# Kernel tuning notes

Measured on AMD Instinct MI355X. Metric: run time of the kernel, lower is better.

Reference implementation:

```python
import jax, jax.numpy as jnp
import numpy as np

N, D, R, DR, H, L = 6000, 128, 1000, 128, 2, 2
MAXN = 1.0 - 4e-3  # Poincare ball projection boundary (c=1)


def _norm(x):
    return jnp.clip(jnp.linalg.norm(x, axis=-1, keepdims=True), 1e-15)


def proj(x):
    n = _norm(x)
    return jnp.where(n > MAXN, x / n * MAXN, x)


def expmap0(u):
    n = _norm(u)
    return proj(jnp.tanh(n) * u / n)


def logmap0(p):
    n = _norm(p)
    return jnp.arctanh(jnp.minimum(n, 1.0 - 1e-7)) * p / n


def mobius_add(x, y):
    x2 = jnp.sum(x * x, -1, keepdims=True)
    y2 = jnp.sum(y * y, -1, keepdims=True)
    xy = jnp.sum(x * y, -1, keepdims=True)
    num = (1 + 2 * xy + y2) * x + (1 - x2) * y
    den = 1 + 2 * xy + x2 * y2
    return num / jnp.clip(den, 1e-15)


def hgc_layer(x, adj, W, b):
    # HypLinear (mobius matvec + hyperbolic bias), HypAgg (tangent-space SpMM), HypAct (relu)
    mv = proj(expmap0(logmap0(x) @ W.T))
    h = proj(mobius_add(mv, proj(expmap0(b))))
    h = proj(expmap0(adj @ logmap0(h)))
    return proj(expmap0(jax.nn.relu(logmap0(h))))


def gat_layer(x, adj, W, a_src, a_dst):
    h = jnp.einsum('nd,hde->hne', x, W)                 # [H,N,D]
    es = jnp.einsum('hne,he->hn', h, a_src)
    ed = jnp.einsum('hne,he->hn', h, a_dst)
    e = jax.nn.leaky_relu(es[:, :, None] + ed[:, None, :], 0.2)  # [H,N,N]
    att = jax.nn.softmax(jnp.where(adj[None] > 0, e, -1e9), axis=-1)
    out = jnp.einsum('hnm,hme->hne', att, h).mean(0)    # head-average -> [N,D]
    return jax.nn.elu(out)


def mha(x, Wq, Wk, Wv, Wfc, g, b):
    # Transformer-style MHA with residual + LayerNorm; x: [N, Lr, D]
    Nn, Lr, _ = x.shape
    split = lambda y: y.reshape(Nn, Lr, H, D).transpose(0, 2, 1, 3)
    q, k, v = split(x @ Wq), split(x @ Wk), split(x @ Wv)
    attn = jax.nn.softmax(jnp.einsum('nhld,nhmd->nhlm', q, k) / jnp.sqrt(jnp.float32(D)), -1)
    o = jnp.einsum('nhlm,nhmd->nhld', attn, v).transpose(0, 2, 1, 3).reshape(Nn, Lr, H * D)
    o = o @ Wfc + x
    mu = o.mean(-1, keepdims=True)
    var = o.var(-1, keepdims=True)
    return g * (o - mu) / jnp.sqrt(var + 1e-6) + b


def _forward(ent_sr, ent_tg, rel_sr, rel_tg, adj_sr, adj_tg, rel_adj_sr, rel_adj_tg,
             gat_W, gat_a_src, gat_a_dst, Wq, Wk, Wv, Wfc, ln_g, ln_b, hgc_W, hgc_b):
    # Relation Aggregator: sparse mm + rowsum normalization
    def rel_agg(radj, remb):
        return (radj @ remb) / radj.sum(-1, keepdims=True)
    sr_rel = rel_agg(rel_adj_sr, rel_sr)
    tg_rel = rel_agg(rel_adj_tg, rel_tg)

    # Attentive Neighbor Aggregator + multi-range fusion (res=True -> range = L+1)
    def branch(x, adj):
        outs, h = [x], x
        for i in range(L):
            h = gat_layer(h, adj, gat_W[i], gat_a_src[i], gat_a_dst[i])
            h = h / jnp.clip(_norm(h), 1e-12)  # F.normalize(dim=1)
            outs.append(h)
        seq = jnp.stack(outs, axis=1)  # [N, L+1, D]
        return mha(seq, Wq, Wk, Wv, Wfc, ln_g, ln_b).mean(1)
    sr = branch(ent_sr, adj_sr)
    tg = branch(ent_tg, adj_tg)

    # Hyperbolic encoder (proj_tan0 is identity for PoincareBall)
    def encode(x, adj):
        h = expmap0(x)
        for i in range(2):
            h = hgc_layer(h, adj, hgc_W[i], hgc_b[i])
        return logmap0(h)
    hs = ent_sr + encode(ent_sr, adj_sr)
    ht = ent_tg + encode(ent_tg, adj_tg)

    return (jnp.concatenate([sr, sr_rel], -1), jnp.concatenate([tg, tg_rel], -1),
            jnp.concatenate([hs, sr_rel], -1), jnp.concatenate([ht, tg_rel], -1))


def setup_inputs() -> dict:
    key = jax.random.key(0)
    ks = jax.random.split(key, 24)

    def make_adj(k):
        m = jax.random.bernoulli(k, 32.0 / N, (N, N)) | jnp.eye(N, dtype=bool)
        a = m.astype(jnp.float32)
        return a / a.sum(-1, keepdims=True)

    def make_rel_adj(k1, k2):
        m = jax.random.bernoulli(k1, 5.0 / R, (N, R)).astype(jnp.float32)
        idx = jax.random.randint(k2, (N,), 0, R)
        return m.at[jnp.arange(N), idx].set(1.0)  # guarantee positive rowsum

    return {
        'ent_sr': 0.02 * jax.random.normal(ks[0], (N, D)),
        'ent_tg': 0.02 * jax.random.normal(ks[1], (N, D)),
        'rel_sr': 0.02 * jax.random.normal(ks[2], (R, DR)),
        'rel_tg': 0.02 * jax.random.normal(ks[3], (R, DR)),
        'adj_sr': make_adj(ks[4]),
        'adj_tg': make_adj(ks[5]),
        'rel_adj_sr': make_rel_adj(ks[6], ks[7]),
        'rel_adj_tg': make_rel_adj(ks[8], ks[9]),
        'gat_W': 0.1 * jax.random.normal(ks[10], (L, H, D, D)),
        'gat_a_src': 0.1 * jax.random.normal(ks[11], (L, H, D)),
        'gat_a_dst': 0.1 * jax.random.normal(ks[12], (L, H, D)),
        'Wq': 0.05 * jax.random.normal(ks[13], (D, H * D)),
        'Wk': 0.05 * jax.random.normal(ks[14], (D, H * D)),
        'Wv': 0.05 * jax.random.normal(ks[15], (D, H * D)),
        'Wfc': 0.05 * jax.random.normal(ks[16], (H * D, D)),
        'ln_g': jnp.ones((D,)),
        'ln_b': jnp.zeros((D,)),
        'hgc_W': 0.05 * jax.random.normal(ks[17], (2, D, D)),
        'hgc_b': 0.01 * jax.random.normal(ks[18], (2, D)),
    }


def reference(ent_sr, ent_tg, rel_sr, rel_tg, adj_sr, adj_tg, rel_adj_sr, rel_adj_tg,
              gat_W, gat_a_src, gat_a_dst, Wq, Wk, Wv, Wfc, ln_g, ln_b, hgc_W, hgc_b):
    return _forward(ent_sr, ent_tg, rel_sr, rel_tg, adj_sr, adj_tg, rel_adj_sr, rel_adj_tg,
                    gat_W, gat_a_src, gat_a_dst, Wq, Wk, Wv, Wfc, ln_g, ln_b, hgc_W, hgc_b)
```

## Files before the change

### kernel.cpp

```cpp
#include <hip/hip_runtime.h>
#include <hip/hip_bf16.h>
#include <math.h>

#define NN   6000
#define N2   12000
#define DD   128
#define RR   1000
#define CAP  96
#define CAPR 48
#define MAXN_F 0.996f

typedef short  bf16x8 __attribute__((ext_vector_type(8)));
typedef float  f32x4  __attribute__((ext_vector_type(4)));

__device__ int      g_dt[19];
__device__ unsigned g_csri[N2 * CAP];
__device__ int      g_cnt[N2];
__device__ float    g_seq[N2 * 3 * DD];
__device__ unsigned short g_seqb[N2 * 3 * DD];
__device__ unsigned short g_hhb[N2 * 256];
__device__ float    g_es[2][N2];
__device__ float    g_ed[2][N2];
__device__ unsigned short g_qkvb[(size_t)N2 * 3 * 768];
__device__ unsigned short g_ob[(size_t)N2 * 3 * 256];
__device__ float    g_fc[N2 * 3 * DD];
__device__ float    g_t[N2 * DD];
__device__ float    g_t2[N2 * DD];
__device__ float    g_hb[2][DD];
__device__ float    g_hb2[2];
__device__ unsigned short g_WgatT[2][256 * DD];
__device__ unsigned short g_WqkvT[768 * DD];
__device__ unsigned short g_WfcT[DD * 256];
__device__ float    g_WhgcT[2][DD * DD];

__device__ __forceinline__ float ldin(const void* p, size_t i, int bf) {
    if (bf) return __uint_as_float(((unsigned)((const unsigned short*)p)[i]) << 16);
    return ((const float*)p)[i];
}
__device__ __forceinline__ unsigned short f2b(float f) {
    unsigned u = __float_as_uint(f);
    u += 0x7FFFu + ((u >> 16) & 1u);
    return (unsigned short)(u >> 16);
}
__device__ __forceinline__ float b2f(unsigned short b) {
    return __uint_as_float(((unsigned)b) << 16);
}
__device__ __forceinline__ float adjval(int c) {
    return b2f(f2b(1.0f / (float)c));
}

__device__ __forceinline__ float wsum(float v) {
    #pragma unroll
// ... 7 lines not shown
}
__device__ __forceinline__ float b128sum(float v, float* r4) {
    v = wsum(v);
    if ((threadIdx.x & 63) == 0) r4[threadIdx.x >> 6] = v;
    __syncthreads();
    float r = r4[0] + r4[1];
    __syncthreads();
    return r;
}
__device__ __forceinline__ void b128sum2(float v0, float v1, float* r4, float& o0, float& o1) {
    v0 = wsum(v0); v1 = wsum(v1);
    int w = threadIdx.x >> 6;
    if ((threadIdx.x & 63) == 0) { r4[w * 2] = v0; r4[w * 2 + 1] = v1; }
    __syncthreads();
    o0 = r4[0] + r4[2]; o1 = r4[1] + r4[3];
    __syncthreads();
}
__device__ __forceinline__ void b128max2(float v0, float v1, float* r4, float& o0, float& o1) {
    v0 = wmax(v0); v1 = wmax(v1);
    int w = threadIdx.x >> 6;
    if ((threadIdx.x & 63) == 0) { r4[w * 2] = v0; r4[w * 2 + 1] = v1; }
    __syncthreads();
    o0 = fmaxf(r4[0], r4[2]); o1 = fmaxf(r4[1], r4[3]);
    __syncthreads();
}

struct P19 { const void* p[19]; };

__global__ void detect_all(P19 ptrs) {
    const int sizes[19] = {768000,768000,128000,128000,36000000,36000000,6000000,6000000,
                           65536,512,512,32768,32768,32768,32768,128,128,32768,256};
    int slot = blockIdx.x;
    const unsigned* p = (const unsigned*)ptrs.p[slot];
    __shared__ int votes[2];
    if (threadIdx.x == 0) { votes[0] = 0; votes[1] = 0; }
    __syncthreads();
    int nwords = sizes[slot] / 2;
    if (nwords > 0) {
        int nsamp = nwords < 4096 ? nwords : 4096;
        int stride = nwords / nsamp; if (stride < 1) stride = 1;
        for (int s = threadIdx.x; s < nsamp; s += blockDim.x) {
            unsigned lo = p[(size_t)s * stride] & 0xFFFFu;
            if (lo) {
                unsigned e = (lo >> 7) & 0xFFu;
                if (e >= 100u && e <= 140u) atomicAdd(&votes[1], 1);
                else                        atomicAdd(&votes[0], 1);
            }
        }
    }
    __syncthreads();
    if (threadIdx.x == 0) g_dt[slot] = (votes[1] > votes[0]) ? 1 : 0;
}

__global__ void prep_weights(const void* gatW, const void* Wq, const void* Wk, const void* Wv,
                             const void* Wfc, const void* hgcW) {
    int stride = gridDim.x * blockDim.x;
    int base = blockIdx.x * blockDim.x + threadIdx.x;
    const int b8 = g_dt[8], b11 = g_dt[11], b12 = g_dt[12], b13 = g_dt[13],
              b14 = g_dt[14], b17 = g_dt[17];
    for (int i = base; i < 65536; i += stride) {
        int e = i & 127, d = (i >> 7) & 127, h = (i >> 14) & 1, l = (i >> 15) & 1;
        g_WgatT[l][(h * 128 + e) * DD + d] = f2b(ldin(gatW, i, b8));
    }
    for (int i = base; i < 32768; i += stride) {
        int d = i >> 8, e = i & 255;
        g_WqkvT[(size_t)e * DD + d]         = f2b(ldin(Wq, i, b11));
        g_WqkvT[(size_t)(256 + e) * DD + d] = f2b(ldin(Wk, i, b12));
        g_WqkvT[(size_t)(512 + e) * DD + d] = f2b(ldin(Wv, i, b13));
    }
    for (int i = base; i < 32768; i += stride) {
        int e = i >> 7, dd = i & 127;
        g_WfcT[dd * 256 + e] = f2b(ldin(Wfc, i, b14));
    }
    for (int i = base; i < 32768; i += stride) {
        int j = i & 127, d = (i >> 7) & 127, l = i >> 14;
        g_WhgcT[l][j * 128 + d] = ldin(hgcW, i, b17);
    }
}

template<bool OUT_BF16>
__global__ __launch_bounds__(256) void gemm_mfma(const unsigned short* __restrict__ A, int lda,
                                                 const unsigned short* __restrict__ Bt, int ldb,
                                                 void* __restrict__ C, int ldc, int M, int K) {
    __shared__ __align__(16) unsigned short As[16 * 128 * 8];
    __shared__ __align__(16) unsigned short Bs[16 * 128 * 8];
    int bm = blockIdx.y * 128, bn = blockIdx.x * 128;
    int tid = threadIdx.x;
    int lane = tid & 63, w = tid >> 6;
    int q = lane >> 4, ln = lane & 15;
    f32x4 acc[8][2] = {};
    for (int k0 = 0; k0 < K; k0 += 128) {
        if (k0 > 0) __syncthreads();
        #pragma unroll
        for (int i = 0; i < 8; i++) {
            int combo = w * 8 + i;
            int c = combo >> 1, half = combo & 1;
            int r = half * 64 + lane;
            int gm = bm + r; if (gm >= M) gm = M - 1;
            *(uint4*)&As[(c * 128 + r) * 8] =
// ... 13 lines not shown
                acc[mt][1] = __builtin_amdgcn_mfma_f32_16x16x32_bf16(af, bf1, acc[mt][1], 0, 0, 0);
            }
        }
    }
    #pragma unroll
    for (int mt = 0; mt < 8; mt++) {
        #pragma unroll
        for (int nt = 0; nt < 2; nt++) {
            int gcol = bn + w * 32 + nt * 16 + ln;
            #pragma unroll
            for (int r = 0; r < 4; r++) {
                int grow = bm + mt * 16 + q * 4 + r;
                if (grow < M) {
                    if (OUT_BF16)
                        ((unsigned short*)C)[(size_t)grow * ldc + gcol] = f2b(acc[mt][nt][r]);
                    else
                        ((float*)C)[(size_t)grow * ldc + gcol] = acc[mt][nt][r];
                }
            }
        }
    }
}

__global__ __launch_bounds__(256) void scan_one(const void* __restrict__ A, int which) {
    int row = (blockIdx.x << 2) | (threadIdx.x >> 6);
    int lane = threadIdx.x & 63;
    if (row >= NN) return;
    int gn = which * NN + row;
    unsigned long long below = (1ull << lane) - 1ull;
    int base = 0;
    if (g_dt[4 + which]) {
        const uint4* p = (const uint4*)((const unsigned short*)A + (size_t)row * NN);
        uint4 cur = p[lane];
        for (int it = 0; it < 12; it++) {
            int idx = it * 64 + lane;
            uint4 nxt = {0u, 0u, 0u, 0u};
            if (it < 11) { int ni = idx + 64; if (ni < 750) nxt = p[ni]; }
            unsigned w4[4] = {cur.x, cur.y, cur.z, cur.w};
            #pragma unroll
            for (int h = 0; h < 4; h++) {
                #pragma unroll
                for (int s = 0; s < 2; s++) {
                    unsigned v16 = s ? (w4[h] >> 16) : (w4[h] & 0xFFFFu);
                    bool pr = v16 && !(v16 & 0x8000u);
                    unsigned long long m = __ballot(pr);
                    if (m) {
                        if (pr) {
                            int pos = base + __popcll(m & below);
                            if (pos < CAP)
                                g_csri[(size_t)gn * CAP + pos] = (unsigned)(idx * 8 + h * 2 + s);
                        }
                        base += __popcll(m);
                    }
                }
            }
            cur = nxt;
        }
    } else {
        const float4* p = (const float4*)((const float*)A + (size_t)row * NN);
        float4 cur = p[lane];
        for (int it = 0; it < 24; it++) {
            int idx = it * 64 + lane;
            float4 nxt = {0.f, 0.f, 0.f, 0.f};
            if (it < 23) { int ni = idx + 64; if (ni < 1500) nxt = p[ni]; }
            float e4[4] = {cur.x, cur.y, cur.z, cur.w};
            #pragma unroll
            for (int h = 0; h < 4; h++) {
                bool pr = e4[h] > 0.f;
                unsigned long long m = __ballot(pr);
                if (m) {
                    if (pr) {
                        int pos = base + __popcll(m & below);
                        if (pos < CAP)
                            g_csri[(size_t)gn * CAP + pos] = (unsigned)(idx * 4 + h);
                    }
                    base += __popcll(m);
                }
            }
            cur = nxt;
        }
    }
    if (lane == 0) g_cnt[gn] = min(base, CAP);
}

__global__ void rel_agg_kernel(const void* __restrict__ ra0, const void* __restrict__ ra1,
                               const void* __restrict__ re0, const void* __restrict__ re1,
                               float* __restrict__ out) {
    int n = blockIdx.x, d = threadIdx.x;
    int which = n >= NN ? 1 : 0;
    const void* radj = which ? ra1 : ra0;
    const void* rel  = which ? re1 : re0;
    const int bfa = g_dt[6 + which], bfr = g_dt[2 + which];
    int row = n - which * NN;
    __shared__ int list[CAPR];
    __shared__ int cs;
    if (d == 0) cs = 0;
    __syncthreads();
    if (bfa) {
        const uint4* p = (const uint4*)((const unsigned short*)radj + (size_t)row * RR);
        for (int i = d; i < RR / 8; i += 128) {
            uint4 w4 = p[i];
            unsigned ws[4] = {w4.x, w4.y, w4.z, w4.w};
            #pragma unroll
            for (int h = 0; h < 4; h++) {
                unsigned lo = ws[h] & 0xFFFFu, hi = ws[h] >> 16;
                if (lo && !(lo & 0x8000u)) { int q = atomicAdd(&cs, 1); if (q < CAPR) list[q] = i * 8 + h * 2; }
                if (hi && !(hi & 0x8000u)) { int q = atomicAdd(&cs, 1); if (q < CAPR) list[q] = i * 8 + h * 2 + 1; }
            }
        }
    } else {
        const float4* p = (const float4*)((const float*)radj + (size_t)row * RR);
        for (int i = d; i < RR / 4; i += 128) {
            float4 w4 = p[i];
            float vs[4] = {w4.x, w4.y, w4.z, w4.w};
            #pragma unroll
            for (int h = 0; h < 4; h++)
                if (vs[h] > 0.f) { int q = atomicAdd(&cs, 1); if (q < CAPR) list[q] = i * 4 + h; }
        }
    }
    __syncthreads();
    int c = min(cs, CAPR);
    float acc = 0.f;
    for (int j = 0; j < c; j++) acc += ldin(rel, (size_t)list[j] * DD + d, bfr);
    float r = c ? acc / (float)c : 0.f;
    out[(size_t)n * 256 + 128 + d] = r;
    out[(size_t)(2 * NN + n) * 256 + 128 + d] = r;
}

__device__ __forceinline__ float hgc_lin_core(float* u, float* r4, int layer, int d) {
    float mv = 0.f;
    #pragma unroll 4
    for (int j = 0; j < DD; j++) mv = fmaf(g_WhgcT[layer][j * 128 + d], u[j], mv);
    float ss2 = b128sum(mv * mv, r4);
    float nm = fmaxf(sqrtf(ss2), 1e-15f);
    float t2 = tanhf(nm);
    float x = t2 / nm * mv;
    float xn = t2;
    if (t2 > MAXN_F) { x *= MAXN_F / t2; xn = MAXN_F; }
    float y = g_hb[layer][d];
    float x2 = xn * xn;
    float y2 = g_hb2[layer];
    float xy = b128sum(x * y, r4);
    float num = (1.f + 2.f * xy + y2) * x + (1.f - x2) * y;
    float den = 1.f + 2.f * xy + x2 * y2;
    den = (fabsf(den) < 1e-15f) ? 1e-15f : den;
    float hv2 = num / den;
    float s3 = b128sum(hv2 * hv2, r4);
    float nn = fmaxf(sqrtf(s3), 1e-15f);
    if (nn > MAXN_F) { hv2 *= MAXN_F / nn; nn = MAXN_F; }
    return atanhf(fminf(nn, 1.f - 1e-7f)) / nn * hv2;
}

__device__ __forceinline__ float hgc_agg_core(const float* tin, int n, int which, float* r4,
                                              int d, unsigned* sidx) {
    int c = min(g_cnt[n], CAP);
    if (d < c)
        sidx[d] = (g_csri[(size_t)n * CAP + d] + (unsigned)(which * NN)) * 128u + (unsigned)d;
    __syncthreads();
    float acc = 0.f;
    int j = 0;
    for (; j + 4 <= c; j += 4) {
        float v0 = tin[(size_t)sidx[j]];
        float v1 = tin[(size_t)sidx[j + 1]];
        float v2 = tin[(size_t)sidx[j + 2]];
        float v3 = tin[(size_t)sidx[j + 3]];
        acc += (v0 + v1) + (v2 + v3);
    }
    for (; j < c; j++) acc += tin[(size_t)sidx[j]];
    acc *= (c > 0) ? adjval(c) : 0.f;
    __syncthreads();
    float ss = b128sum(acc * acc, r4);
    float nm = fmaxf(sqrtf(ss), 1e-15f);
    float t = tanhf(nm);
    float x = t / nm * acc;
    float xn = t;
    if (t > MAXN_F) { x *= MAXN_F / t; xn = MAXN_F; }
    float u = atanhf(fminf(xn, 1.f - 1e-7f)) / fmaxf(xn, 1e-15f) * x;
    u = fmaxf(u, 0.f);
    float ss2 = b128sum(u * u, r4);
    float nm2 = fmaxf(sqrtf(ss2), 1e-15f);
    float t2 = tanhf(nm2);
    float x2 = t2 / nm2 * u;
    float xn2 = t2;
    if (t2 > MAXN_F) { x2 *= MAXN_F / t2; xn2 = MAXN_F; }
    return atanhf(fminf(xn2, 1.f - 1e-7f)) / fmaxf(xn2, 1e-15f) * x2;
}

__global__ void hgc_bias(const void* __restrict__ hgc_b) {
    int i = blockIdx.x, d = threadIdx.x;
    __shared__ float r4[4];
    float bv = ldin(hgc_b, (size_t)i * DD + d, g_dt[18]);
    float ss = b128sum(bv * bv, r4);
    float nrm = fmaxf(sqrtf(ss), 1e-15f);
    float t = tanhf(nrm);
    float v = t / nrm * bv;
    float vn = t;
    if (t > MAXN_F) { v *= MAXN_F / t; vn = MAXN_F; }
    g_hb[i][d] = v;
    if (d == 0) g_hb2[i] = vn * vn;
}

__global__ void ent_init(const void* __restrict__ e0, const void* __restrict__ e1) {
    int n = blockIdx.x, d = threadIdx.x;
    int which = n >= NN ? 1 : 0;
    __shared__ float r4[4];
    __shared__ float u[128];
    float x = ldin(which ? e1 : e0, (size_t)(n - which * NN) * DD + d, g_dt[which]);
    g_seq[(size_t)n * 384 + d] = x;
    g_seqb[(size_t)n * 384 + d] = f2b(x);
    float ss = b128sum(x * x, r4);
    float nrm = fmaxf(sqrtf(ss), 1e-15f);
    float t = tanhf(nrm);
    float scale = t / nrm;
    float hn = t;
    if (t > MAXN_F) { scale *= MAXN_F / t; hn = MAXN_F; }
    u[d] = atanhf(fminf(hn, 1.f - 1e-7f)) / fmaxf(hn, 1e-15f) * (scale * x);
    __syncthreads();
    g_t[(size_t)n * DD + d] = hgc_lin_core(u, r4, 0, d);
}

__global__ __launch_bounds__(256) void gat_scores(int layer, const void* __restrict__ a_src,
                                                  const void* __restrict__ a_dst) {
    int n = blockIdx.x, tid = threadIdx.x;
    int h = tid >> 7, e = tid & 127;
    const int bfs = g_dt[9], bfd = g_dt[10];
    __shared__ float r8[8];
    float hv = b2f(g_hhb[(size_t)n * 256 + tid]);
    size_t abase = ((size_t)layer * 2 + h) * DD;
    float vs = wsum(hv * ldin(a_src, abase + e, bfs));
    float vd = wsum(hv * ldin(a_dst, abase + e, bfd));
    int w = tid >> 6;
    if ((tid & 63) == 0) { r8[w * 2] = vs; r8[w * 2 + 1] = vd; }
    __syncthreads();
    if (tid == 0)   { g_es[0][n] = r8[0] + r8[2]; g_ed[0][n] = r8[1] + r8[3]; }
    if (tid == 128) { g_es[1][n] = r8[4] + r8[6]; g_ed[1][n] = r8[5] + r8[7]; }
}

__global__ void gat_attn(int layer) {
    int n = blockIdx.x, d = threadIdx.x;
    int which = n >= NN ? 1 : 0;
    int c = min(g_cnt[n], CAP);
    __shared__ float w0s[CAP], w1s[CAP];
    __shared__ unsigned bases[CAP];
// ... 31 lines not shown
        accHi = fmaf(g1, b2f((unsigned short)(v1 >> 16)), accHi);
        accLo = fmaf(g2, b2f((unsigned short)(v2 & 0xFFFFu)), accLo);
        accHi = fmaf(g2, b2f((unsigned short)(v2 >> 16)), accHi);
        accLo = fmaf(g3, b2f((unsigned short)(v3 & 0xFFFFu)), accLo);
        accHi = fmaf(g3, b2f((unsigned short)(v3 >> 16)), accHi);
    }
    for (; j < c; j++) {
        unsigned wv = hh32[(size_t)bases[j] + d];
        float wgt = wsrc[j];
        accLo = fmaf(wgt, b2f((unsigned short)(wv & 0xFFFFu)), accLo);
        accHi = fmaf(wgt, b2f((unsigned short)(wv >> 16)), accHi);
    }
    sh[2 * d] = accLo; sh[2 * d + 1] = accHi;
    __syncthreads();
    float o = (c > 0) ? 0.5f * (sh[d] + sh[128 + d]) : 0.f;
    o = o > 0.f ? o : expm1f(o);
    __syncthreads();
    float ss = b128sum(o * o, r4);
    float r = o / fmaxf(sqrtf(ss), 1e-12f);
    g_seq[(size_t)n * 384 + (layer + 1) * 128 + d] = r;
    g_seqb[(size_t)n * 384 + (layer + 1) * 128 + d] = f2b(r);
}

__global__ __launch_bounds__(256) void mha_attn() {
    int n = blockIdx.x, tid = threadIdx.x;
    __shared__ float qs[3][256], ks[3][256], vs[3][256], os[3][256];
    __shared__ float att[2][3][3];
    const unsigned* src = (const unsigned*)(g_qkvb + (size_t)n * 3 * 768);
    for (int t = tid; t < 1152; t += 256) {
        unsigned wv = src[t];
        int l = t / 384, r = t - l * 384;
        int sec = r >> 7, e2 = (r & 127) * 2;
        float f0 = b2f((unsigned short)(wv & 0xFFFFu));
        float f1 = b2f((unsigned short)(wv >> 16));
        float* dstp = (sec == 0) ? qs[l] : (sec == 1) ? ks[l] : vs[l];
        dstp[e2] = f0; dstp[e2 + 1] = f1;
    }
    __syncthreads();
    if (tid < 144) {
        int g = tid >> 3, sub = tid & 7;
        int h = g / 9, lm = g % 9, l = lm / 3, m = lm % 3;
        int d0 = h * 128 + sub * 16;
        float acc = 0.f;
        #pragma unroll
        for (int k = 0; k < 16; k++) acc += qs[l][d0 + k] * ks[m][d0 + k];
        #pragma unroll
        for (int o = 1; o < 8; o <<= 1) acc += __shfl_xor(acc, o, 8);
        if (sub == 0) att[h][l][m] = acc * 0.08838834764831845f;
    }
    __syncthreads();
    if (tid < 6) {
        int h = tid / 3, l = tid % 3;
        float mx = fmaxf(att[h][l][0], fmaxf(att[h][l][1], att[h][l][2]));
        float e0 = expf(att[h][l][0] - mx), e1 = expf(att[h][l][1] - mx), e2 = expf(att[h][l][2] - mx);
        float s = fmaxf(e0 + e1 + e2, 1e-30f);
        att[h][l][0] = e0 / s; att[h][l][1] = e1 / s; att[h][l][2] = e2 / s;
    }
    __syncthreads();
    for (int t = tid; t < 768; t += 256) {
        int l = t >> 8, e = t & 255, h = e >> 7;
        os[l][e] = att[h][l][0] * vs[0][e] + att[h][l][1] * vs[1][e] + att[h][l][2] * vs[2][e];
    }
    __syncthreads();
    unsigned* dst = (unsigned*)(g_ob + (size_t)n * 3 * 256);
    for (int t = tid; t < 384; t += 256) {
        int l = t / 128, e2 = (t % 128) * 2;
        dst[t] = (unsigned)f2b(os[l][e2]) | ((unsigned)f2b(os[l][e2 + 1]) << 16);
    }
}

__global__ void mha_out(const void* __restrict__ g, const void* __restrict__ b,
                        float* __restrict__ out) {
    int n = blockIdx.x, d = threadIdx.x;
    const int bg = g_dt[15], bb = g_dt[16];
    __shared__ float r4[4];
    float ool[3], mu[3], rstd[3];
    #pragma unroll
    for (int l = 0; l < 3; l++)
        ool[l] = g_fc[(size_t)(n * 3 + l) * 128 + d] + g_seq[(size_t)(n * 3 + l) * 128 + d];
    #pragma unroll
    for (int l = 0; l < 3; l++) {
        float s, ss;
        b128sum2(ool[l], ool[l] * ool[l], r4, s, ss);
        mu[l] = s / 128.f;
        rstd[l] = rsqrtf(ss / 128.f - mu[l] * mu[l] + 1e-6f);
    }
    float acc = 0.f;
    #pragma unroll
    for (int l = 0; l < 3; l++) acc += (ool[l] - mu[l]) * rstd[l];
    out[(size_t)n * 256 + d] = ldin(g, d, bg) * (acc / 3.f) + ldin(b, d, bb);
}

__global__ void hgc_mid() {
    int n = blockIdx.x, d = threadIdx.x;
    int which = n >= NN ? 1 : 0;
    __shared__ float r4[4];
    __shared__ float u[128];
    __shared__ unsigned sidx[CAP];
    float u3 = hgc_agg_core(g_t, n, which, r4, d, sidx);
    u[d] = u3;
    __syncthreads();
    g_t2[(size_t)n * DD + d] = hgc_lin_core(u, r4, 1, d);
}

__global__ void hgc_fin(const void* __restrict__ e0, const void* __restrict__ e1,
                        float* __restrict__ out) {
    int n = blockIdx.x, d = threadIdx.x;
    int which = n >= NN ? 1 : 0;
    __shared__ float r4[4];
    __shared__ unsigned sidx[CAP];
    float u3 = hgc_agg_core(g_t2, n, which, r4, d, sidx);
    float ev = ldin(which ? e1 : e0, (size_t)(n - which * NN) * DD + d, g_dt[which]);
    out[(size_t)(2 * NN + n) * 256 + d] = ev + u3;
}

extern "C" void kernel_launch(void* const* d_in, const int* in_sizes, int n_in,
                              void* d_out, int out_size, void* d_ws, size_t ws_size,
                              hipStream_t stream) {
    const void* ent_sr = d_in[0];
    const void* ent_tg = d_in[1];
    const void* rel_sr = d_in[2];
    const void* rel_tg = d_in[3];
    const void* adj_sr = d_in[4];
    const void* adj_tg = d_in[5];
    const void* rel_adj_sr = d_in[6];
    const void* rel_adj_tg = d_in[7];
    const void* gat_W     = d_in[8];
    const void* gat_a_src = d_in[9];
    const void* gat_a_dst = d_in[10];
    const void* Wq  = d_in[11];
    const void* Wk  = d_in[12];
    const void* Wv  = d_in[13];
    const void* Wfc = d_in[14];
    const void* ln_g = d_in[15];
    const void* ln_b = d_in[16];
    const void* hgc_W = d_in[17];
    const void* hgc_b = d_in[18];

    float* out = (float*)d_out;

    unsigned short *p_seqb, *p_hhb, *p_qkvb, *p_ob, *p_WgatT, *p_WqkvT, *p_WfcT;
    float *p_fc;
    hipGetSymbolAddress((void**)&p_seqb,  HIP_SYMBOL(g_seqb));
    hipGetSymbolAddress((void**)&p_hhb,   HIP_SYMBOL(g_hhb));
    hipGetSymbolAddress((void**)&p_qkvb,  HIP_SYMBOL(g_qkvb));
    hipGetSymbolAddress((void**)&p_ob,    HIP_SYMBOL(g_ob));
    hipGetSymbolAddress((void**)&p_WgatT, HIP_SYMBOL(g_WgatT));
    hipGetSymbolAddress((void**)&p_WqkvT, HIP_SYMBOL(g_WqkvT));
    hipGetSymbolAddress((void**)&p_WfcT,  HIP_SYMBOL(g_WfcT));
    hipGetSymbolAddress((void**)&p_fc,    HIP_SYMBOL(g_fc));

    P19 ptrs;
    for (int i = 0; i < 19; i++) ptrs.p[i] = d_in[i];
    detect_all<<<19, 256, 0, stream>>>(ptrs);

    scan_one<<<NN / 4, 256, 0, stream>>>(adj_sr, 0);

    prep_weights<<<128, 256, 0, stream>>>(gat_W, Wq, Wk, Wv, Wfc, hgc_W);
    rel_agg_kernel<<<N2, 128, 0, stream>>>(rel_adj_sr, rel_adj_tg, rel_sr, rel_tg, out);
    hgc_bias<<<2, 128, 0, stream>>>(hgc_b);
    ent_init<<<N2, 128, 0, stream>>>(ent_sr, ent_tg);

    gemm_mfma<true><<<dim3(2, 94), 256, 0, stream>>>(
        p_seqb, 384, p_WgatT, DD, p_hhb, 256, N2, 128);
    gat_scores<<<N2, 256, 0, stream>>>(0, gat_a_src, gat_a_dst);

    scan_one<<<NN / 4, 256, 0, stream>>>(adj_tg, 1);

    gat_attn<<<N2, 128, 0, stream>>>(0);
    gemm_mfma<true><<<dim3(2, 94), 256, 0, stream>>>(
        p_seqb + 128, 384, p_WgatT + (size_t)256 * DD, DD, p_hhb, 256, N2, 128);
    gat_scores<<<N2, 256, 0, stream>>>(1, gat_a_src, gat_a_dst);
    gat_attn<<<N2, 128, 0, stream>>>(1);

    gemm_mfma<true><<<dim3(6, 282), 256, 0, stream>>>(
        p_seqb, 128, p_WqkvT, DD, p_qkvb, 768, N2 * 3, 128);
    mha_attn<<<N2, 256, 0, stream>>>();
    gemm_mfma<false><<<dim3(1, 282), 256, 0, stream>>>(
        p_ob, 256, p_WfcT, 256, p_fc, 128, N2 * 3, 256);
    mha_out<<<N2, 128, 0, stream>>>(ln_g, ln_b, out);

    hgc_mid<<<N2, 128, 0, stream>>>();
    hgc_fin<<<N2, 128, 0, stream>>>(ent_sr, ent_tg, out);
}
```

Measured before the change: 707.5 us.

## Merge independent front, attention and HGC stages into horizontally fused mega-kernels

Combines the adjacency scans, relation aggregation, entity init, first HGC linear layer and weight prep into one block-partitioned kernel. The MHA attention is merged with the second HGC aggregation/linear stage, and the LayerNorm output with the final HGC aggregation. HGC work now packs two nodes per 256-thread block and computes the hyperbolic bias inline instead of in a separate kernel. The aim is fewer launches and better overlap of independent work, at the cost of heavier blocks, more shared memory per block, and redundant bias computation in every block.

```diff
diff --git a/kernel.cpp b/kernel.cpp
--- a/kernel.cpp
+++ b/kernel.cpp
@@ -26,8 +26,6 @@
 __device__ float    g_fc[N2 * 3 * DD];
 __device__ float    g_t[N2 * DD];
 __device__ float    g_t2[N2 * DD];
-__device__ float    g_hb[2][DD];
-__device__ float    g_hb2[2];
 __device__ unsigned short g_WgatT[2][256 * DD];
 __device__ unsigned short g_WqkvT[768 * DD];
 __device__ unsigned short g_WfcT[DD * 256];
@@ -81,6 +79,26 @@
     if ((threadIdx.x & 63) == 0) { r4[w * 2] = v0; r4[w * 2 + 1] = v1; }
     __syncthreads();
     o0 = fmaxf(r4[0], r4[2]); o1 = fmaxf(r4[1], r4[3]);
+    __syncthreads();
+}
+__device__ __forceinline__ float h128sum(float v, float* r8) {
+    v = wsum(v);
+    int w = threadIdx.x >> 6;
+    if ((threadIdx.x & 63) == 0) r8[w] = v;
+    __syncthreads();
+    int h = threadIdx.x >> 7;
+    float r = r8[2 * h] + r8[2 * h + 1];
+    __syncthreads();
+    return r;
+}
+__device__ __forceinline__ void h128sum2(float v0, float v1, float* r8, float& o0, float& o1) {
+    v0 = wsum(v0); v1 = wsum(v1);
+    int w = threadIdx.x >> 6;
+    if ((threadIdx.x & 63) == 0) { r8[w * 2] = v0; r8[w * 2 + 1] = v1; }
+    __syncthreads();
+    int h = threadIdx.x >> 7;
+    o0 = r8[4 * h] + r8[4 * h + 2];
+    o1 = r8[4 * h + 1] + r8[4 * h + 3];
     __syncthreads();
 }
 
@@ -111,29 +129,224 @@
     if (threadIdx.x == 0) g_dt[slot] = (votes[1] > votes[0]) ? 1 : 0;
 }
 
-__global__ void prep_weights(const void* gatW, const void* Wq, const void* Wk, const void* Wv,
-                             const void* Wfc, const void* hgcW) {
-    int stride = gridDim.x * blockDim.x;
-    int base = blockIdx.x * blockDim.x + threadIdx.x;
-    const int b8 = g_dt[8], b11 = g_dt[11], b12 = g_dt[12], b13 = g_dt[13],
-              b14 = g_dt[14], b17 = g_dt[17];
-    for (int i = base; i < 65536; i += stride) {
-        int e = i & 127, d = (i >> 7) & 127, h = (i >> 14) & 1, l = (i >> 15) & 1;
-        g_WgatT[l][(h * 128 + e) * DD + d] = f2b(ldin(gatW, i, b8));
-    }
-    for (int i = base; i < 32768; i += stride) {
-        int d = i >> 8, e = i & 255;
-        g_WqkvT[(size_t)e * DD + d]         = f2b(ldin(Wq, i, b11));
-        g_WqkvT[(size_t)(256 + e) * DD + d] = f2b(ldin(Wk, i, b12));
-        g_WqkvT[(size_t)(512 + e) * DD + d] = f2b(ldin(Wv, i, b13));
-    }
-    for (int i = base; i < 32768; i += stride) {
-        int e = i >> 7, dd = i & 127;
-        g_WfcT[dd * 256 + e] = f2b(ldin(Wfc, i, b14));
-    }
-    for (int i = base; i < 32768; i += stride) {
-        int j = i & 127, d = (i >> 7) & 127, l = i >> 14;
-        g_WhgcT[l][j * 128 + d] = ldin(hgcW, i, b17);
+__device__ __forceinline__ float bias_inline(const void* hgc_b, int layer, int d, float* r8,
+                                             float& y2) {
+    float bv = ldin(hgc_b, (size_t)layer * DD + d, g_dt[18]);
+    float ss = h128sum(bv * bv, r8);
+    float nrm = fmaxf(sqrtf(ss), 1e-15f);
+    float t = tanhf(nrm);
+    float v = t / nrm * bv;
+    float vn = t;
+    if (t > MAXN_F) { v *= MAXN_F / t; vn = MAXN_F; }
+    y2 = vn * vn;
+    return v;
+}
+
+__device__ __forceinline__ float hgc_lin_h(const float* uh, float* r8, int layer, int d,
+                                           float y, float y2) {
+    float mv = 0.f;
+    #pragma unroll 4
+    for (int j = 0; j < DD; j++) mv = fmaf(g_WhgcT[layer][j * 128 + d], uh[j], mv);
+    float ss2 = h128sum(mv * mv, r8);
+    float nm = fmaxf(sqrtf(ss2), 1e-15f);
+    float t2 = tanhf(nm);
+    float x = t2 / nm * mv;
+    float xn = t2;
+    if (t2 > MAXN_F) { x *= MAXN_F / t2; xn = MAXN_F; }
+    float x2 = xn * xn;
+    float xy = h128sum(x * y, r8);
+    float num = (1.f + 2.f * xy + y2) * x + (1.f - x2) * y;
+    float den = 1.f + 2.f * xy + x2 * y2;
+    den = (fabsf(den) < 1e-15f) ? 1e-15f : den;
+    float hv2 = num / den;
+    float s3 = h128sum(hv2 * hv2, r8);
+    float nn = fmaxf(sqrtf(s3), 1e-15f);
+    if (nn > MAXN_F) { hv2 *= MAXN_F / nn; nn = MAXN_F; }
+    return atanhf(fminf(nn, 1.f - 1e-7f)) / nn * hv2;
+}
+
+__device__ __forceinline__ float hgc_agg_h(const float* tin, int n, int which, float* r8,
+                                           int d, unsigned* sidxh) {
+    int c = min(g_cnt[n], CAP);
+    if (d < c)
+        sidxh[d] = (g_csri[(size_t)n * CAP + d] + (unsigned)(which * NN)) * 128u + (unsigned)d;
+    __syncthreads();
+    float acc = 0.f;
+    int j = 0;
+    for (; j + 4 <= c; j += 4) {
+        float v0 = tin[(size_t)sidxh[j]];
+        float v1 = tin[(size_t)sidxh[j + 1]];
+        float v2 = tin[(size_t)sidxh[j + 2]];
+        float v3 = tin[(size_t)sidxh[j + 3]];
+        acc += (v0 + v1) + (v2 + v3);
+    }
+    for (; j < c; j++) acc += tin[(size_t)sidxh[j]];
+    acc *= (c > 0) ? adjval(c) : 0.f;
+    __syncthreads();
+    float ss = h128sum(acc * acc, r8);
+    float nm = fmaxf(sqrtf(ss), 1e-15f);
+    float t = tanhf(nm);
+    float x = t / nm * acc;
+    float xn = t;
+    if (t > MAXN_F) { x *= MAXN_F / t; xn = MAXN_F; }
+    float u = atanhf(fminf(xn, 1.f - 1e-7f)) / fmaxf(xn, 1e-15f) * x;
+    u = fmaxf(u, 0.f);
+    float ss2 = h128sum(u * u, r8);
+    float nm2 = fmaxf(sqrtf(ss2), 1e-15f);
+    float t2 = tanhf(nm2);
+    float x2 = t2 / nm2 * u;
+    float xn2 = t2;
+    if (t2 > MAXN_F) { x2 *= MAXN_F / t2; xn2 = MAXN_F; }
+    return atanhf(fminf(xn2, 1.f - 1e-7f)) / fmaxf(xn2, 1e-15f) * x2;
+}
+
+__global__ __launch_bounds__(256) void front_mega(P19 in, float* __restrict__ out) {
+    int b = blockIdx.x;
+    int tid = threadIdx.x;
+    if (b < 3000) {
+        int which = b >= 1500 ? 1 : 0;
+        int row = ((which ? b - 1500 : b) << 2) | (tid >> 6);
+        int lane = tid & 63;
+        const void* A = in.p[4 + which];
+        int gn = which * NN + row;
+        unsigned long long below = (1ull << lane) - 1ull;
+        int base = 0;
+        if (g_dt[4 + which]) {
+            const uint4* p = (const uint4*)((const unsigned short*)A + (size_t)row * NN);
+            uint4 cur = p[lane];
+            for (int it = 0; it < 12; it++) {
+                int idx = it * 64 + lane;
+                uint4 nxt = {0u, 0u, 0u, 0u};
+                if (it < 11) { int ni = idx + 64; if (ni < 750) nxt = p[ni]; }
+                unsigned w4[4] = {cur.x, cur.y, cur.z, cur.w};
+                #pragma unroll
+                for (int h = 0; h < 4; h++) {
+                    #pragma unroll
+                    for (int s = 0; s < 2; s++) {
+                        unsigned v16 = s ? (w4[h] >> 16) : (w4[h] & 0xFFFFu);
+                        bool pr = v16 && !(v16 & 0x8000u);
+                        unsigned long long m = __ballot(pr);
+                        if (m) {
+                            if (pr) {
+                                int pos = base + __popcll(m & below);
+                                if (pos < CAP)
+                                    g_csri[(size_t)gn * CAP + pos] = (unsigned)(idx * 8 + h * 2 + s);
+                            }
+                            base += __popcll(m);
+                        }
+                    }
+                }
+                cur = nxt;
+            }
+        } else {
+            const float4* p = (const float4*)((const float*)A + (size_t)row * NN);
+            float4 cur = p[lane];
+            for (int it = 0; it < 24; it++) {
+                int idx = it * 64 + lane;
+                float4 nxt = {0.f, 0.f, 0.f, 0.f};
+                if (it < 23) { int ni = idx + 64; if (ni < 1500) nxt = p[ni]; }
+                float e4[4] = {cur.x, cur.y, cur.z, cur.w};
+                #pragma unroll
+                for (int h = 0; h < 4; h++) {
+                    bool pr = e4[h] > 0.f;
+                    unsigned long long m = __ballot(pr);
+                    if (m) {
+                        if (pr) {
+                            int pos = base + __popcll(m & below);
+                            if (pos < CAP)
+                                g_csri[(size_t)gn * CAP + pos] = (unsigned)(idx * 4 + h);
+                        }
+                        base += __popcll(m);
+                    }
+                }
+                cur = nxt;
+            }
+        }
+        if (lane == 0) g_cnt[gn] = min(base, CAP);
+    } else if (b < 9000) {
+        int half = tid >> 7, d = tid & 127;
+        int n = (b - 3000) * 2 + half;
+        int which = n >= NN ? 1 : 0;
+        const void* radj = in.p[6 + which];
+        const void* rel  = in.p[2 + which];
+        const int bfa = g_dt[6 + which], bfr = g_dt[2 + which];
+        int row = n - which * NN;
+        __shared__ int list[2][CAPR];
+        __shared__ int cs[2];
+        if (d == 0) cs[half] = 0;
+        __syncthreads();
+        if (bfa) {
+            const uint4* p = (const uint4*)((const unsigned short*)radj + (size_t)row * RR);
+            if (d < RR / 8) {
+                uint4 w4 = p[d];
+                unsigned ws[4] = {w4.x, w4.y, w4.z, w4.w};
+                #pragma unroll
+                for (int h = 0; h < 4; h++) {
+                    unsigned lo = ws[h] & 0xFFFFu, hi = ws[h] >> 16;
+                    if (lo && !(lo & 0x8000u)) { int q = atomicAdd(&cs[half], 1); if (q < CAPR) list[half][q] = d * 8 + h * 2; }
+                    if (hi && !(hi & 0x8000u)) { int q = atomicAdd(&cs[half], 1); if (q < CAPR) list[half][q] = d * 8 + h * 2 + 1; }
+                }
+            }
+        } else {
+            const float4* p = (const float4*)((const float*)radj + (size_t)row * RR);
+            for (int i = d; i < RR / 4; i += 128) {
+                float4 w4 = p[i];
+                float vs[4] = {w4.x, w4.y, w4.z, w4.w};
+                #pragma unroll
+                for (int h = 0; h < 4; h++)
+                    if (vs[h] > 0.f) { int q = atomicAdd(&cs[half], 1); if (q < CAPR) list[half][q] = i * 4 + h; }
+            }
+        }
+        __syncthreads();
+        int c = min(cs[half], CAPR);
+        float acc = 0.f;
+        for (int j = 0; j < c; j++) acc += ldin(rel, (size_t)list[half][j] * DD + d, bfr);
+        float r = c ? acc / (float)c : 0.f;
+        out[(size_t)n * 256 + 128 + d] = r;
+        out[(size_t)(2 * NN + n) * 256 + 128 + d] = r;
+    } else if (b < 15000) {
+        int half = tid >> 7, d = tid & 127;
+        int n = (b - 9000) * 2 + half;
+        int which = n >= NN ? 1 : 0;
+        __shared__ float r8[8];
+        __shared__ float u[2][128];
+        float y02;
+        float y0 = bias_inline(in.p[18], 0, d, r8, y02);
+        float x = ldin(in.p[which], (size_t)(n - which * NN) * DD + d, g_dt[which]);
+        g_seq[(size_t)n * 384 + d] = x;
+        g_seqb[(size_t)n * 384 + d] = f2b(x);
+        float ss = h128sum(x * x, r8);
+        float nrm = fmaxf(sqrtf(ss), 1e-15f);
+        float t = tanhf(nrm);
+        float scale = t / nrm;
+        float hn = t;
+        if (t > MAXN_F) { scale *= MAXN_F / t; hn = MAXN_F; }
+        u[half][d] = atanhf(fminf(hn, 1.f - 1e-7f)) / fmaxf(hn, 1e-15f) * (scale * x);
+        __syncthreads();
+        g_t[(size_t)n * DD + d] = hgc_lin_h(u[half], r8, 0, d, y0, y02);
+    } else {
+        int stride = 128 * 256;
+        int base = (b - 15000) * 256 + tid;
+        const int b8 = g_dt[8], b11 = g_dt[11], b12 = g_dt[12], b13 = g_dt[13],
+                  b14 = g_dt[14], b17 = g_dt[17];
+        for (int i = base; i < 65536; i += stride) {
+            int e = i & 127, d = (i >> 7) & 127, h = (i >> 14) & 1, l = (i >> 15) & 1;
+            g_WgatT[l][(h * 128 + e) * DD + d] = f2b(ldin(in.p[8], i, b8));
+        }
+        for (int i = base; i < 32768; i += stride) {
+            int d = i >> 8, e = i & 255;
+            g_WqkvT[(size_t)e * DD + d]         = f2b(ldin(in.p[11], i, b11));
+            g_WqkvT[(size_t)(256 + e) * DD + d] = f2b(ldin(in.p[12], i, b12));
+            g_WqkvT[(size_t)(512 + e) * DD + d] = f2b(ldin(in.p[13], i, b13));
+        }
+        for (int i = base; i < 32768; i += stride) {
+            int e = i >> 7, dd = i & 127;
+            g_WfcT[dd * 256 + e] = f2b(ldin(in.p[14], i, b14));
+        }
+        for (int i = base; i < 32768; i += stride) {
+            int j = i & 127, d = (i >> 7) & 127, l = i >> 14;
+            g_WhgcT[l][j * 128 + d] = ldin(in.p[17], i, b17);
+        }
     }
 }
 
@@ -193,203 +406,6 @@
     }
 }
 
-__global__ __launch_bounds__(256) void scan_one(const void* __restrict__ A, int which) {
-    int row = (blockIdx.x << 2) | (threadIdx.x >> 6);
-    int lane = threadIdx.x & 63;
-    if (row >= NN) return;
-    int gn = which * NN + row;
-    unsigned long long below = (1ull << lane) - 1ull;
-    int base = 0;
-    if (g_dt[4 + which]) {
-        const uint4* p = (const uint4*)((const unsigned short*)A + (size_t)row * NN);
-        uint4 cur = p[lane];
-        for (int it = 0; it < 12; it++) {
-            int idx = it * 64 + lane;
-            uint4 nxt = {0u, 0u, 0u, 0u};
-            if (it < 11) { int ni = idx + 64; if (ni < 750) nxt = p[ni]; }
-            unsigned w4[4] = {cur.x, cur.y, cur.z, cur.w};
-            #pragma unroll
-            for (int h = 0; h < 4; h++) {
-                #pragma unroll
-                for (int s = 0; s < 2; s++) {
-                    unsigned v16 = s ? (w4[h] >> 16) : (w4[h] & 0xFFFFu);
-                    bool pr = v16 && !(v16 & 0x8000u);
-                    unsigned long long m = __ballot(pr);
-                    if (m) {
-                        if (pr) {
-                            int pos = base + __popcll(m & below);
-                            if (pos < CAP)
-                                g_csri[(size_t)gn * CAP + pos] = (unsigned)(idx * 8 + h * 2 + s);
-                        }
-                        base += __popcll(m);
-                    }
-                }
-            }
-            cur = nxt;
-        }
-    } else {
-        const float4* p = (const float4*)((const float*)A + (size_t)row * NN);
-        float4 cur = p[lane];
-        for (int it = 0; it < 24; it++) {
-            int idx = it * 64 + lane;
-            float4 nxt = {0.f, 0.f, 0.f, 0.f};
-            if (it < 23) { int ni = idx + 64; if (ni < 1500) nxt = p[ni]; }
-            float e4[4] = {cur.x, cur.y, cur.z, cur.w};
-            #pragma unroll
-            for (int h = 0; h < 4; h++) {
-                bool pr = e4[h] > 0.f;
-                unsigned long long m = __ballot(pr);
-                if (m) {
-                    if (pr) {
-                        int pos = base + __popcll(m & below);
-                        if (pos < CAP)
-                            g_csri[(size_t)gn * CAP + pos] = (unsigned)(idx * 4 + h);
-                    }
-                    base += __popcll(m);
-                }
-            }
-            cur = nxt;
-        }
-    }
-    if (lane == 0) g_cnt[gn] = min(base, CAP);
-}
-
-__global__ void rel_agg_kernel(const void* __restrict__ ra0, const void* __restrict__ ra1,
-                               const void* __restrict__ re0, const void* __restrict__ re1,
-                               float* __restrict__ out) {
-    int n = blockIdx.x, d = threadIdx.x;
-    int which = n >= NN ? 1 : 0;
-    const void* radj = which ? ra1 : ra0;
-    const void* rel  = which ? re1 : re0;
-    const int bfa = g_dt[6 + which], bfr = g_dt[2 + which];
-    int row = n - which * NN;
-    __shared__ int list[CAPR];
-    __shared__ int cs;
-    if (d == 0) cs = 0;
-    __syncthreads();
-    if (bfa) {
-        const uint4* p = (const uint4*)((const unsigned short*)radj + (size_t)row * RR);
-        for (int i = d; i < RR / 8; i += 128) {
-            uint4 w4 = p[i];
-            unsigned ws[4] = {w4.x, w4.y, w4.z, w4.w};
-            #pragma unroll
-            for (int h = 0; h < 4; h++) {
-                unsigned lo = ws[h] & 0xFFFFu, hi = ws[h] >> 16;
-                if (lo && !(lo & 0x8000u)) { int q = atomicAdd(&cs, 1); if (q < CAPR) list[q] = i * 8 + h * 2; }
-                if (hi && !(hi & 0x8000u)) { int q = atomicAdd(&cs, 1); if (q < CAPR) list[q] = i * 8 + h * 2 + 1; }
-            }
-        }
-    } else {
-        const float4* p = (const float4*)((const float*)radj + (size_t)row * RR);
-        for (int i = d; i < RR / 4; i += 128) {
-            float4 w4 = p[i];
-            float vs[4] = {w4.x, w4.y, w4.z, w4.w};
-            #pragma unroll
-            for (int h = 0; h < 4; h++)
-                if (vs[h] > 0.f) { int q = atomicAdd(&cs, 1); if (q < CAPR) list[q] = i * 4 + h; }
-        }
-    }
-    __syncthreads();
-    int c = min(cs, CAPR);
-    float acc = 0.f;
-    for (int j = 0; j < c; j++) acc += ldin(rel, (size_t)list[j] * DD + d, bfr);
-    float r = c ? acc / (float)c : 0.f;
-    out[(size_t)n * 256 + 128 + d] = r;
-    out[(size_t)(2 * NN + n) * 256 + 128 + d] = r;
-}
-
-__device__ __forceinline__ float hgc_lin_core(float* u, float* r4, int layer, int d) {
-    float mv = 0.f;
-    #pragma unroll 4
-    for (int j = 0; j < DD; j++) mv = fmaf(g_WhgcT[layer][j * 128 + d], u[j], mv);
-    float ss2 = b128sum(mv * mv, r4);
-    float nm = fmaxf(sqrtf(ss2), 1e-15f);
-    float t2 = tanhf(nm);
-    float x = t2 / nm * mv;
-    float xn = t2;
-    if (t2 > MAXN_F) { x *= MAXN_F / t2; xn = MAXN_F; }
-    float y = g_hb[layer][d];
-    float x2 = xn * xn;
-    float y2 = g_hb2[layer];
-    float xy = b128sum(x * y, r4);
-    float num = (1.f + 2.f * xy + y2) * x + (1.f - x2) * y;
-    float den = 1.f + 2.f * xy + x2 * y2;
-    den = (fabsf(den) < 1e-15f) ? 1e-15f : den;
-    float hv2 = num / den;
-    float s3 = b128sum(hv2 * hv2, r4);
-    float nn = fmaxf(sqrtf(s3), 1e-15f);
-    if (nn > MAXN_F) { hv2 *= MAXN_F / nn; nn = MAXN_F; }
-    return atanhf(fminf(nn, 1.f - 1e-7f)) / nn * hv2;
-}
-
-__device__ __forceinline__ float hgc_agg_core(const float* tin, int n, int which, float* r4,
-                                              int d, unsigned* sidx) {
-    int c = min(g_cnt[n], CAP);
-    if (d < c)
-        sidx[d] = (g_csri[(size_t)n * CAP + d] + (unsigned)(which * NN)) * 128u + (unsigned)d;
-    __syncthreads();
-    float acc = 0.f;
-    int j = 0;
-    for (; j + 4 <= c; j += 4) {
-        float v0 = tin[(size_t)sidx[j]];
-        float v1 = tin[(size_t)sidx[j + 1]];
-        float v2 = tin[(size_t)sidx[j + 2]];
-        float v3 = tin[(size_t)sidx[j + 3]];
-        acc += (v0 + v1) + (v2 + v3);
-    }
-    for (; j < c; j++) acc += tin[(size_t)sidx[j]];
-    acc *= (c > 0) ? adjval(c) : 0.f;
-    __syncthreads();
-    float ss = b128sum(acc * acc, r4);
-    float nm = fmaxf(sqrtf(ss), 1e-15f);
-    float t = tanhf(nm);
-    float x = t / nm * acc;
-    float xn = t;
-    if (t > MAXN_F) { x *= MAXN_F / t; xn = MAXN_F; }
-    float u = atanhf(fminf(xn, 1.f - 1e-7f)) / fmaxf(xn, 1e-15f) * x;
-    u = fmaxf(u, 0.f);
-    float ss2 = b128sum(u * u, r4);
-    float nm2 = fmaxf(sqrtf(ss2), 1e-15f);
-    float t2 = tanhf(nm2);
-    float x2 = t2 / nm2 * u;
-    float xn2 = t2;
-    if (t2 > MAXN_F) { x2 *= MAXN_F / t2; xn2 = MAXN_F; }
-    return atanhf(fminf(xn2, 1.f - 1e-7f)) / fmaxf(xn2, 1e-15f) * x2;
-}
-
-__global__ void hgc_bias(const void* __restrict__ hgc_b) {
-    int i = blockIdx.x, d = threadIdx.x;
-    __shared__ float r4[4];
-    float bv = ldin(hgc_b, (size_t)i * DD + d, g_dt[18]);
-    float ss = b128sum(bv * bv, r4);
-    float nrm = fmaxf(sqrtf(ss), 1e-15f);
-    float t = tanhf(nrm);
-    float v = t / nrm * bv;
-    float vn = t;
-    if (t > MAXN_F) { v *= MAXN_F / t; vn = MAXN_F; }
-    g_hb[i][d] = v;
-    if (d == 0) g_hb2[i] = vn * vn;
-}
-
-__global__ void ent_init(const void* __restrict__ e0, const void* __restrict__ e1) {
-    int n = blockIdx.x, d = threadIdx.x;
-    int which = n >= NN ? 1 : 0;
-    __shared__ float r4[4];
-    __shared__ float u[128];
-    float x = ldin(which ? e1 : e0, (size_t)(n - which * NN) * DD + d, g_dt[which]);
-    g_seq[(size_t)n * 384 + d] = x;
-    g_seqb[(size_t)n * 384 + d] = f2b(x);
-    float ss = b128sum(x * x, r4);
-    float nrm = fmaxf(sqrtf(ss), 1e-15f);
-    float t = tanhf(nrm);
-    float scale = t / nrm;
-    float hn = t;
-    if (t > MAXN_F) { scale *= MAXN_F / t; hn = MAXN_F; }
-    u[d] = atanhf(fminf(hn, 1.f - 1e-7f)) / fmaxf(hn, 1e-15f) * (scale * x);
-    __syncthreads();
-    g_t[(size_t)n * DD + d] = hgc_lin_core(u, r4, 0, d);
-}
-
 __global__ __launch_bounds__(256) void gat_scores(int layer, const void* __restrict__ a_src,
                                                   const void* __restrict__ a_dst) {
     int n = blockIdx.x, tid = threadIdx.x;
@@ -467,119 +483,111 @@
     g_seqb[(size_t)n * 384 + (layer + 1) * 128 + d] = f2b(r);
 }
 
-__global__ __launch_bounds__(256) void mha_attn() {
-    int n = blockIdx.x, tid = threadIdx.x;
-    __shared__ float qs[3][256], ks[3][256], vs[3][256], os[3][256];
-    __shared__ float att[2][3][3];
-    const unsigned* src = (const unsigned*)(g_qkvb + (size_t)n * 3 * 768);
-    for (int t = tid; t < 1152; t += 256) {
-        unsigned wv = src[t];
-        int l = t / 384, r = t - l * 384;
-        int sec = r >> 7, e2 = (r & 127) * 2;
-        float f0 = b2f((unsigned short)(wv & 0xFFFFu));
-        float f1 = b2f((unsigned short)(wv >> 16));
-        float* dstp = (sec == 0) ? qs[l] : (sec == 1) ? ks[l] : vs[l];
-        dstp[e2] = f0; dstp[e2 + 1] = f1;
-    }
-    __syncthreads();
-    if (tid < 144) {
-        int g = tid >> 3, sub = tid & 7;
-        int h = g / 9, lm = g % 9, l = lm / 3, m = lm % 3;
-        int d0 = h * 128 + sub * 16;
+__global__ __launch_bounds__(256) void attn_mid(const void* __restrict__ hgc_b) {
+    int tid = threadIdx.x;
+    if (blockIdx.x < N2) {
+        int n = blockIdx.x;
+        __shared__ float qs[3][256], ks[3][256], vs[3][256], os[3][256];
+        __shared__ float att[2][3][3];
+        const unsigned* src = (const unsigned*)(g_qkvb + (size_t)n * 3 * 768);
+        for (int t = tid; t < 1152; t += 256) {
+            unsigned wv = src[t];
+            int l = t / 384, r = t - l * 384;
+            int sec = r >> 7, e2 = (r & 127) * 2;
+            float f0 = b2f((unsigned short)(wv & 0xFFFFu));
+            float f1 = b2f((unsigned short)(wv >> 16));
+            float* dstp = (sec == 0) ? qs[l] : (sec == 1) ? ks[l] : vs[l];
+            dstp[e2] = f0; dstp[e2 + 1] = f1;
+        }
+        __syncthreads();
+        if (tid < 144) {
+            int g = tid >> 3, sub = tid & 7;
+            int h = g / 9, lm = g % 9, l = lm / 3, m = lm % 3;
+            int d0 = h * 128 + sub * 16;
+            float acc = 0.f;
+            #pragma unroll
+            for (int k = 0; k < 16; k++) acc += qs[l][d0 + k] * ks[m][d0 + k];
+            #pragma unroll
+            for (int o = 1; o < 8; o <<= 1) acc += __shfl_xor(acc, o, 8);
+            if (sub == 0) att[h][l][m] = acc * 0.08838834764831845f;
+        }
+        __syncthreads();
+        if (tid < 6) {
+            int h = tid / 3, l = tid % 3;
+            float mx = fmaxf(att[h][l][0], fmaxf(att[h][l][1], att[h][l][2]));
+            float e0 = expf(att[h][l][0] - mx), e1 = expf(att[h][l][1] - mx), e2 = expf(att[h][l][2] - mx);
+            float s = fmaxf(e0 + e1 + e2, 1e-30f);
+            att[h][l][0] = e0 / s; att[h][l][1] = e1 / s; att[h][l][2] = e2 / s;
+        }
+        __syncthreads();
+        for (int t = tid; t < 768; t += 256) {
+            int l = t >> 8, e = t & 255, h = e >> 7;
+            os[l][e] = att[h][l][0] * vs[0][e] + att[h][l][1] * vs[1][e] + att[h][l][2] * vs[2][e];
+        }
+        __syncthreads();
+        unsigned* dst = (unsigned*)(g_ob + (size_t)n * 3 * 256);
+        for (int t = tid; t < 384; t += 256) {
+            int l = t / 128, e2 = (t % 128) * 2;
+            dst[t] = (unsigned)f2b(os[l][e2]) | ((unsigned)f2b(os[l][e2 + 1]) << 16);
+        }
+    } else {
+        int half = tid >> 7, d = tid & 127;
+        int n = (blockIdx.x - N2) * 2 + half;
+        int which = n >= NN ? 1 : 0;
+        __shared__ float r8[8];
+        __shared__ float u2[2][128];
+        __shared__ unsigned sidx[2][CAP];
+        float y12;
+        float y1 = bias_inline(hgc_b, 1, d, r8, y12);
+        float u3 = hgc_agg_h(g_t, n, which, r8, d, sidx[half]);
+        u2[half][d] = u3;
+        __syncthreads();
+        g_t2[(size_t)n * DD + d] = hgc_lin_h(u2[half], r8, 1, d, y1, y12);
+    }
+}
+
+__global__ __launch_bounds__(256) void out_fin(const void* __restrict__ g, const void* __restrict__ b,
+                                               const void* __restrict__ e0, const void* __restrict__ e1,
+                                               float* __restrict__ out) {
+    int tid = threadIdx.x;
+    int half = tid >> 7, d = tid & 127;
+    if (blockIdx.x < 6000) {
+        int n = blockIdx.x * 2 + half;
+        const int bg = g_dt[15], bb = g_dt[16];
+        __shared__ float r8[8];
+        float ool[3], mu[3], rstd[3];
+        #pragma unroll
+        for (int l = 0; l < 3; l++)
+            ool[l] = g_fc[(size_t)(n * 3 + l) * 128 + d] + g_seq[(size_t)(n * 3 + l) * 128 + d];
+        #pragma unroll
+        for (int l = 0; l < 3; l++) {
+            float s, ss;
+            h128sum2(ool[l], ool[l] * ool[l], r8, s, ss);
+            mu[l] = s / 128.f;
+            rstd[l] = rsqrtf(ss / 128.f - mu[l] * mu[l] + 1e-6f);
+        }
         float acc = 0.f;
         #pragma unroll
-        for (int k = 0; k < 16; k++) acc += qs[l][d0 + k] * ks[m][d0 + k];
-        #pragma unroll
-        for (int o = 1; o < 8; o <<= 1) acc += __shfl_xor(acc, o, 8);
-        if (sub == 0) att[h][l][m] = acc * 0.08838834764831845f;
-    }
-    __syncthreads();
-    if (tid < 6) {
-        int h = tid / 3, l = tid % 3;
-        float mx = fmaxf(att[h][l][0], fmaxf(att[h][l][1], att[h][l][2]));
-        float e0 = expf(att[h][l][0] - mx), e1 = expf(att[h][l][1] - mx), e2 = expf(att[h][l][2] - mx);
-        float s = fmaxf(e0 + e1 + e2, 1e-30f);
-        att[h][l][0] = e0 / s; att[h][l][1] = e1 / s; att[h][l][2] = e2 / s;
-    }
-    __syncthreads();
-    for (int t = tid; t < 768; t += 256) {
-        int l = t >> 8, e = t & 255, h = e >> 7;
-        os[l][e] = att[h][l][0] * vs[0][e] + att[h][l][1] * vs[1][e] + att[h][l][2] * vs[2][e];
-    }
-    __syncthreads();
-    unsigned* dst = (unsigned*)(g_ob + (size_t)n * 3 * 256);
-    for (int t = tid; t < 384; t += 256) {
-        int l = t / 128, e2 = (t % 128) * 2;
-        dst[t] = (unsigned)f2b(os[l][e2]) | ((unsigned)f2b(os[l][e2 + 1]) << 16);
-    }
-}
-
-__global__ void mha_out(const void* __restrict__ g, const void* __restrict__ b,
-                        float* __restrict__ out) {
-    int n = blockIdx.x, d = threadIdx.x;
-    const int bg = g_dt[15], bb = g_dt[16];
-    __shared__ float r4[4];
-    float ool[3], mu[3], rstd[3];
-    #pragma unroll
-    for (int l = 0; l < 3; l++)
-        ool[l] = g_fc[(size_t)(n * 3 + l) * 128 + d] + g_seq[(size_t)(n * 3 + l) * 128 + d];
-    #pragma unroll
-    for (int l = 0; l < 3; l++) {
-        float s, ss;
-        b128sum2(ool[l], ool[l] * ool[l], r4, s, ss);
-        mu[l] = s / 128.f;
-        rstd[l] = rsqrtf(ss / 128.f - mu[l] * mu[l] + 1e-6f);
-    }
-    float acc = 0.f;
-    #pragma unroll
-    for (int l = 0; l < 3; l++) acc += (ool[l] - mu[l]) * rstd[l];
-    out[(size_t)n * 256 + d] = ldin(g, d, bg) * (acc / 3.f) + ldin(b, d, bb);
-}
-
-__global__ void hgc_mid() {
-    int n = blockIdx.x, d = threadIdx.x;
-    int which = n >= NN ? 1 : 0;
-    __shared__ float r4[4];
-    __shared__ float u[128];
-    __shared__ unsigned sidx[CAP];
-    float u3 = hgc_agg_core(g_t, n, which, r4, d, sidx);
-    u[d] = u3;
-    __syncthreads();
-    g_t2[(size_t)n * DD + d] = hgc_lin_core(u, r4, 1, d);
-}
-
-__global__ void hgc_fin(const void* __restrict__ e0, const void* __restrict__ e1,
-                        float* __restrict__ out) {
-    int n = blockIdx.x, d = threadIdx.x;
-    int which = n >= NN ? 1 : 0;
-    __shared__ float r4[4];
-    __shared__ unsigned sidx[CAP];
-    float u3 = hgc_agg_core(g_t2, n, which, r4, d, sidx);
-    float ev = ldin(which ? e1 : e0, (size_t)(n - which * NN) * DD + d, g_dt[which]);
-    out[(size_t)(2 * NN + n) * 256 + d] = ev + u3;
+        for (int l = 0; l < 3; l++) acc += (ool[l] - mu[l]) * rstd[l];
+        out[(size_t)n * 256 + d] = ldin(g, d, bg) * (acc / 3.f) + ldin(b, d, bb);
+    } else {
+        int n = (blockIdx.x - 6000) * 2 + half;
+        int which = n >= NN ? 1 : 0;
+        __shared__ float r8[8];
+        __shared__ unsigned sidx[2][CAP];
+        float u3 = hgc_agg_h(g_t2, n, which, r8, d, sidx[half]);
+        float ev = ldin(which ? e1 : e0, (size_t)(n - which * NN) * DD + d, g_dt[which]);
+        out[(size_t)(2 * NN + n) * 256 + d] = ev + u3;
+    }
 }
 
 extern "C" void kernel_launch(void* const* d_in, const int* in_sizes, int n_in,
                               void* d_out, int out_size, void* d_ws, size_t ws_size,
                               hipStream_t stream) {
-    const void* ent_sr = d_in[0];
-    const void* ent_tg = d_in[1];
-    const void* rel_sr = d_in[2];
-    const void* rel_tg = d_in[3];
-    const void* adj_sr = d_in[4];
-    const void* adj_tg = d_in[5];
-    const void* rel_adj_sr = d_in[6];
-    const void* rel_adj_tg = d_in[7];
-    const void* gat_W     = d_in[8];
     const void* gat_a_src = d_in[9];
     const void* gat_a_dst = d_in[10];
-    const void* Wq  = d_in[11];
-    const void* Wk  = d_in[12];
-    const void* Wv  = d_in[13];
-    const void* Wfc = d_in[14];
     const void* ln_g = d_in[15];
     const void* ln_b = d_in[16];
-    const void* hgc_W = d_in[17];
     const void* hgc_b = d_in[18];
 
     float* out = (float*)d_out;
@@ -599,19 +607,11 @@
     for (int i = 0; i < 19; i++) ptrs.p[i] = d_in[i];
     detect_all<<<19, 256, 0, stream>>>(ptrs);
 
-    scan_one<<<NN / 4, 256, 0, stream>>>(adj_sr, 0);
-
-    prep_weights<<<128, 256, 0, stream>>>(gat_W, Wq, Wk, Wv, Wfc, hgc_W);
-    rel_agg_kernel<<<N2, 128, 0, stream>>>(rel_adj_sr, rel_adj_tg, rel_sr, rel_tg, out);
-    hgc_bias<<<2, 128, 0, stream>>>(hgc_b);
-    ent_init<<<N2, 128, 0, stream>>>(ent_sr, ent_tg);
+    front_mega<<<15128, 256, 0, stream>>>(ptrs, out);
 
     gemm_mfma<true><<<dim3(2, 94), 256, 0, stream>>>(
         p_seqb, 384, p_WgatT, DD, p_hhb, 256, N2, 128);
     gat_scores<<<N2, 256, 0, stream>>>(0, gat_a_src, gat_a_dst);
-
-    scan_one<<<NN / 4, 256, 0, stream>>>(adj_tg, 1);
-
     gat_attn<<<N2, 128, 0, stream>>>(0);
     gemm_mfma<true><<<dim3(2, 94), 256, 0, stream>>>(
         p_seqb + 128, 384, p_WgatT + (size_t)256 * DD, DD, p_hhb, 256, N2, 128);
@@ -620,11 +620,8 @@
 
     gemm_mfma<true><<<dim3(6, 282), 256, 0, stream>>>(
         p_seqb, 128, p_WqkvT, DD, p_qkvb, 768, N2 * 3, 128);
-    mha_attn<<<N2, 256, 0, stream>>>();
+    attn_mid<<<N2 + 6000, 256, 0, stream>>>(hgc_b);
     gemm_mfma<false><<<dim3(1, 282), 256, 0, stream>>>(
         p_ob, 256, p_WfcT, 256, p_fc, 128, N2 * 3, 256);
-    mha_out<<<N2, 128, 0, stream>>>(ln_g, ln_b, out);
-
-    hgc_mid<<<N2, 128, 0, stream>>>();
-    hgc_fin<<<N2, 128, 0, stream>>>(ent_sr, ent_tg, out);
-}
+    out_fin<<<12000, 256, 0, stream>>>(ln_g, ln_b, d_in[0], d_in[1], out);
+}
```

New measurement: 683.7 us. -3.4%, faster.
